# Performance work log

Measured on AMD Instinct MI355X. Metric: run time of the kernel, lower is better.

Reference implementation:

```python
import jax, jax.numpy as jnp
import numpy as np

N_NODES = 100000
N_EDGES = 3200000
F_IN = 128
F_OUT = 128


def setup_inputs() -> dict:
    key = jax.random.key(0)
    ks = jax.random.split(key, 6)
    stdv = 1.0 / np.sqrt(F_OUT)
    return {
        "x": jax.random.normal(ks[0], (N_NODES, F_IN), dtype=jnp.float32),
        "weight": jax.random.uniform(ks[1], (F_IN, F_OUT), minval=-stdv, maxval=stdv, dtype=jnp.float32),
        "bias": jax.random.uniform(ks[2], (F_OUT,), minval=-stdv, maxval=stdv, dtype=jnp.float32),
        "edge_src": jax.random.randint(ks[3], (N_EDGES,), 0, N_NODES, dtype=jnp.int32),
        "edge_dst": jax.random.randint(ks[4], (N_EDGES,), 0, N_NODES, dtype=jnp.int32),
        "edge_weight": jax.random.uniform(ks[5], (N_EDGES,), dtype=jnp.float32),
    }


def reference(x, weight, bias, edge_src, edge_dst, edge_weight):
    # Dense feature transform: support = X @ W  -> [N, F_OUT]
    support = jnp.matmul(x, weight)
    # Sparse adjacency aggregation (SpMM): out[d] = sum_e A[d, s_e] * support[s_e]
    msgs = support[edge_src] * edge_weight[:, None]  # [E, F_OUT]
    out = jax.ops.segment_sum(msgs, edge_dst, num_segments=N_NODES)
    return out + bias
```

## Files before the change

### kernel.cpp

```cpp
#include <hip/hip_runtime.h>

#define F 128
#define NB 64
#define MAXB 2048
#define NCHUNK 256
#define BCAP 3072

typedef __bf16 bf16x8 __attribute__((ext_vector_type(8)));
typedef unsigned short u16x8 __attribute__((ext_vector_type(8)));
typedef float f32x4 __attribute__((ext_vector_type(4)));

static __device__ __forceinline__ unsigned short f2bf(float f) {
    unsigned u = __float_as_uint(f);
    unsigned r = (u + 0x7FFF + ((u >> 16) & 1)) >> 16;
    return (unsigned short)r;
}

__global__ __launch_bounds__(256) void gemm_mfma_kernel(const float* __restrict__ X,
                                                        const float* __restrict__ W,
                                                        unsigned short* __restrict__ Sb,
                                                        int n_nodes) {
    __shared__ unsigned short WT[F * F];
    int t = threadIdx.x;
    {
        int f = t >> 1, half = t & 1;
#pragma unroll
        for (int j = 0; j < 8; ++j) {
            int k0 = half * 64 + j * 8;
            u16x8 pk;
#pragma unroll
            for (int i = 0; i < 8; ++i) pk[i] = f2bf(W[(size_t)(k0 + i) * F + f]);
            int byte = f * 256 + ((k0 * 2) ^ ((f & 7) << 4));
            *(u16x8*)((char*)WT + byte) = pk;
        }
    }
    __syncthreads();

    int w = t >> 6, l = t & 63;
    int lr = l & 15, lg = l >> 4;
    int rowBase = blockIdx.x * 128 + w * 32;

    f32x4 acc[2][8] = {};
    int r0 = rowBase + lr;
    int r1 = rowBase + 16 + lr;
    if (r0 >= n_nodes) r0 = n_nodes - 1;
    if (r1 >= n_nodes) r1 = n_nodes - 1;
    const float* a0p = X + (size_t)r0 * F + lg * 8;
    const float* a1p = X + (size_t)r1 * F + lg * 8;

#pragma unroll
    for (int kt = 0; kt < 4; ++kt) {
        float4 x0 = *(const float4*)(a0p + kt * 32);
        float4 x1 = *(const float4*)(a0p + kt * 32 + 4);
        u16x8 au;
        au[0] = f2bf(x0.x); au[1] = f2bf(x0.y); au[2] = f2bf(x0.z); au[3] = f2bf(x0.w);
        au[4] = f2bf(x1.x); au[5] = f2bf(x1.y); au[6] = f2bf(x1.z); au[7] = f2bf(x1.w);
        bf16x8 a0 = __builtin_bit_cast(bf16x8, au);
        float4 y0 = *(const float4*)(a1p + kt * 32);
        float4 y1 = *(const float4*)(a1p + kt * 32 + 4);
        au[0] = f2bf(y0.x); au[1] = f2bf(y0.y); au[2] = f2bf(y0.z); au[3] = f2bf(y0.w);
        au[4] = f2bf(y1.x); au[5] = f2bf(y1.y); au[6] = f2bf(y1.z); au[7] = f2bf(y1.w);
        bf16x8 a1 = __builtin_bit_cast(bf16x8, au);
#pragma unroll
        for (int ct = 0; ct < 8; ++ct) {
            int f = ct * 16 + lr;
            int byte = f * 256 + (((kt * 32 + lg * 8) * 2) ^ ((f & 7) << 4));
            bf16x8 b = *(bf16x8*)((char*)WT + byte);
            acc[0][ct] = __builtin_amdgcn_mfma_f32_16x16x32_bf16(a0, b, acc[0][ct], 0, 0, 0);
            acc[1][ct] = __builtin_amdgcn_mfma_f32_16x16x32_bf16(a1, b, acc[1][ct], 0, 0, 0);
        }
    }

#pragma unroll
    for (int tile = 0; tile < 2; ++tile) {
#pragma unroll
        for (int ct = 0; ct < 8; ++ct) {
            int col = ct * 16 + lr;
#pragma unroll
            for (int j = 0; j < 4; ++j) {
                int row = rowBase + tile * 16 + lg * 4 + j;
                if (row < n_nodes) Sb[(size_t)row * F + col] = f2bf(acc[tile][ct][j]);
            }
        }
    }
}

__global__ __launch_bounds__(256) void chunk_hist_kernel(const int* __restrict__ edst,
                                                         int* __restrict__ counts,
                                                         int* __restrict__ bcnt,
                                                         int n_edges, int nbuck, int epc) {
    __shared__ int h[MAXB];
    int c = blockIdx.x, t = threadIdx.x;
    for (int i = t; i < nbuck; i += 256) h[i] = 0;
    __syncthreads();
    int beg = c * epc, end = min(n_edges, beg + epc);
    for (int e = beg + t; e < end; e += 256) {
        atomicAdd(&h[edst[e] >> 6], 1);
    }
    __syncthreads();
    for (int i = t; i < nbuck; i += 256) {
        int v = h[i];
        counts[(size_t)c * nbuck + i] = v;
        if (v) __hip_atomic_fetch_add(&bcnt[i], v, __ATOMIC_RELAXED, __HIP_MEMORY_SCOPE_AGENT);
    }
}

__global__ __launch_bounds__(256) void bscan_kernel(const int* __restrict__ bcnt,
                                                    int* __restrict__ bstart, int nbuck) {
    __shared__ int tsum[256];
    int t = threadIdx.x;
    const int EPT = MAXB / 256;
    int base = t * EPT;
    int v[EPT];
    int s = 0;
#pragma unroll
    for (int i = 0; i < EPT; ++i) {
        int idx = base + i;
        v[i] = (idx < nbuck) ? bcnt[idx] : 0;
        s += v[i];
    }
    tsum[t] = s;
    __syncthreads();
    for (int off = 1; off < 256; off <<= 1) {
        int x = (t >= off) ? tsum[t - off] : 0;
        __syncthreads();
        tsum[t] += x;
        __syncthreads();
    }
    int run = tsum[t] - s;
#pragma unroll
    for (int i = 0; i < EPT; ++i) {
        int idx = base + i;
        if (idx < nbuck) {
            bstart[idx] = run;
            run += v[i];
        }
    }
    if (t == 255) bstart[nbuck] = run;
}

__global__ __launch_bounds__(256) void chunk_offs_kernel(const int* __restrict__ counts,
                                                         const int* __restrict__ bstart,
                                                         int* __restrict__ offs, int nbuck) {
    __shared__ int part[4][64];
    int t = threadIdx.x;
    int q = t >> 6, bb = t & 63;
    int b = blockIdx.x * 64 + bb;
    int s = 0;
    if (b < nbuck) {
        for (int c = q * 64; c < q * 64 + 64; ++c) s += counts[(size_t)c * nbuck + b];
    }
    part[q][bb] = s;
    __syncthreads();
    if (b < nbuck) {
        int run = bstart[b];
        for (int qq = 0; qq < q; ++qq) run += part[qq][bb];
        for (int c = q * 64; c < q * 64 + 64; ++c) {
            size_t idx = (size_t)c * nbuck + b;
            offs[idx] = run;
            run += counts[idx];
        }
    }
}

__global__ __launch_bounds__(256) void chunk_scatter_kernel(const int* __restrict__ esrc,
                                                            const int* __restrict__ edst,
                                                            const float* __restrict__ ew,
                                                            const int* __restrict__ offs,
                                                            int2* __restrict__ ebuf,
                                                            int n_edges, int nbuck, int epc) {
    __shared__ int lcur[MAXB];
    int c = blockIdx.x, t = threadIdx.x;
    for (int i = t; i < nbuck; i += 256) lcur[i] = offs[(size_t)c * nbuck + i];
    __syncthreads();
    int beg = c * epc, end = min(n_edges, beg + epc);
    for (int e = beg + t; e < end; e += 256) {
        int d = edst[e];
        int pos = atomicAdd(&lcur[d >> 6], 1);
        int2 p;
        p.x = esrc[e] | ((d & (NB - 1)) << 20);
        p.y = __float_as_int(ew[e]);
        ebuf[pos] = p;
    }
}

__global__ __launch_bounds__(256) void local_sort_kernel(const int2* __restrict__ ebuf,
                                                         const int* __restrict__ bstart,
                                                         unsigned* __restrict__ csr,
                                                         int* __restrict__ rowst,
                                                         int* __restrict__ cnt_out, int n_nodes) {
    __shared__ int lcnt[NB];
    __shared__ int lcur[NB];
    __shared__ int2 se[BCAP];
    int b = blockIdx.x, t = threadIdx.x;
    int beg = bstart[b], end = bstart[b + 1];
    int num = end - beg;
    bool inl = num <= BCAP;

    if (t < NB) lcnt[t] = 0;
    __syncthreads();

    for (int i = t; i < num; i += 256) {
        int2 p = ebuf[beg + i];
        if (inl) se[i] = p;
        atomicAdd(&lcnt[(p.x >> 20) & (NB - 1)], 1);
    }
    __syncthreads();

    if (t < NB) {
        int v = lcnt[t];
        int inc = v;
#pragma unroll
        for (int off = 1; off < NB; off <<= 1) {
            int up = __shfl_up(inc, off, NB);
            if (t >= off) inc += up;
        }
        int excl = inc - v;
        lcur[t] = excl;
        int node = b * NB + t;
        if (node < n_nodes) {
            rowst[node] = beg + excl;
            cnt_out[node] = v;
        }
    }
    __syncthreads();

    for (int i = t; i < num; i += 256) {
        int2 p = inl ? se[i] : ebuf[beg + i];
        int dl = (p.x >> 20) & (NB - 1);
        int pos = beg + atomicAdd(&lcur[dl], 1);
        float wv = __int_as_float(p.y);
        unsigned wfix = (unsigned)(wv * 4095.0f + 0.5f);
        if (wfix > 4095u) wfix = 4095u;
        csr[pos] = (unsigned)(p.x & 0xFFFFF) | (wfix << 20);
    }
}

__global__ __launch_bounds__(256) void gather_kernel(const unsigned short* __restrict__ Sb,
                                                     const unsigned* __restrict__ csr,
                                                     const int* __restrict__ rowst,
                                                     const int* __restrict__ cnt,
                                                     const float* __restrict__ bias,
                                                     float* __restrict__ out, int n_nodes) {
    int node = blockIdx.x * 4 + (threadIdx.x >> 6);
    if (node >= n_nodes) return;
    int lane = threadIdx.x & 63;
    int half = lane >> 5, l32 = lane & 31;

    int beg = rowst[node];
    int num = cnt[node];
    int last = beg + num - 1;

    float4 acc = {0.f, 0.f, 0.f, 0.f};
    const unsigned short* sbp = Sb + l32 * 4;
    const float WSCALE = 1.0f / 4095.0f;

    int i = 0;
    for (; i + 16 <= num; i += 16) {
        unsigned long long g[8];
        float wt[8];
#pragma unroll
        for (int j = 0; j < 8; ++j) {
            unsigned p = csr[beg + i + 2 * j + half];
            g[j] = *(const unsigned long long*)(sbp + (size_t)(p & 0xFFFFFu) * F);
            wt[j] = (float)(p >> 20) * WSCALE;
        }
#pragma unroll
        for (int j = 0; j < 8; ++j) {
            unsigned lo = (unsigned)g[j], hi = (unsigned)(g[j] >> 32);
            acc.x += wt[j] * __uint_as_float(lo << 16);
            acc.y += wt[j] * __uint_as_float(lo & 0xFFFF0000u);
            acc.z += wt[j] * __uint_as_float(hi << 16);
            acc.w += wt[j] * __uint_as_float(hi & 0xFFFF0000u);
        }
    }
    for (; i < num; i += 2) {
        bool live = (i + half) < num;
        unsigned p = csr[live ? beg + i + half : last];
        float wt = live ? (float)(p >> 20) * WSCALE : 0.f;
        unsigned long long g = *(const unsigned long long*)(sbp + (size_t)(p & 0xFFFFFu) * F);
        unsigned lo = (unsigned)g, hi = (unsigned)(g >> 32);
        acc.x += wt * __uint_as_float(lo << 16);
        acc.y += wt * __uint_as_float(lo & 0xFFFF0000u);
        acc.z += wt * __uint_as_float(hi << 16);
        acc.w += wt * __uint_as_float(hi & 0xFFFF0000u);
    }

    acc.x += __shfl_xor(acc.x, 32);
    acc.y += __shfl_xor(acc.y, 32);
    acc.z += __shfl_xor(acc.z, 32);
    acc.w += __shfl_xor(acc.w, 32);

    if (half == 0) {
        float4 bi = *(const float4*)&bias[l32 * 4];
        acc.x += bi.x; acc.y += bi.y; acc.z += bi.z; acc.w += bi.w;
        *(float4*)&out[(size_t)node * F + l32 * 4] = acc;
    }
}

__global__ __launch_bounds__(256) void init_out_kernel(float* __restrict__ out,
                                                       const float* __restrict__ bias,
                                                       int n_nodes) {
    int idx = blockIdx.x * blockDim.x + threadIdx.x;
    int total = n_nodes * F;
    if (idx < total) out[idx] = bias[idx & (F - 1)];
}

__global__ __launch_bounds__(256) void scatter_edges_kernel(const unsigned short* __restrict__ Sb,
                                                            const int* __restrict__ esrc,
                                                            const int* __restrict__ edst,
                                                            const float* __restrict__ ew,
                                                            float* __restrict__ out,
                                                            int n_edges) {
    long long idx = (long long)blockIdx.x * blockDim.x + threadIdx.x;
    int e = (int)(idx >> 5);
    if (e >= n_edges) return;
    int fbase = ((int)idx & 31) * 4;
    int s = esrc[e];
    int d = edst[e];
    float w = ew[e];
    ushort4 v = *(const ushort4*)&Sb[(size_t)s * F + fbase];
    float* o = out + (size_t)d * F + fbase;
    __hip_atomic_fetch_add(&o[0], w * __uint_as_float((unsigned)v.x << 16), __ATOMIC_RELAXED, __HIP_MEMORY_SCOPE_AGENT);
    __hip_atomic_fetch_add(&o[1], w * __uint_as_float((unsigned)v.y << 16), __ATOMIC_RELAXED, __HIP_MEMORY_SCOPE_AGENT);
    __hip_atomic_fetch_add(&o[2], w * __uint_as_float((unsigned)v.z << 16), __ATOMIC_RELAXED, __HIP_MEMORY_SCOPE_AGENT);
    __hip_atomic_fetch_add(&o[3], w * __uint_as_float((unsigned)v.w << 16), __ATOMIC_RELAXED, __HIP_MEMORY_SCOPE_AGENT);
}

extern "C" void kernel_launch(void* const* d_in, const int* in_sizes, int n_in,
                              void* d_out, int out_size, void* d_ws, size_t ws_size,
                              hipStream_t stream) {
    const float* x    = (const float*)d_in[0];
    const float* w    = (const float*)d_in[1];
    const float* bias = (const float*)d_in[2];
    const int*   esrc = (const int*)d_in[3];
    const int*   edst = (const int*)d_in[4];
    const float* ew   = (const float*)d_in[5];
    float* out = (float*)d_out;

    int n_nodes = in_sizes[0] / F;
    int n_edges = in_sizes[3];
    int nbuck = (n_nodes + NB - 1) / NB;
    int epc = (n_edges + NCHUNK - 1) / NCHUNK;

    size_t off = 0;
    auto carve = [&](size_t bytes) -> void* {
        void* p = (char*)d_ws + off;
        off += (bytes + 255) & ~(size_t)255;
        return p;
    };
    unsigned short* Sb    = (unsigned short*)carve((size_t)n_nodes * F * sizeof(unsigned short));
    int2*           ebuf  = (int2*)carve((size_t)n_edges * sizeof(int2));
    unsigned*       csr   = (unsigned*)carve((size_t)n_edges * sizeof(unsigned));
    int*            bcnt  = (int*)carve((size_t)nbuck * sizeof(int));
    int*            bst   = (int*)carve((size_t)(nbuck + 1) * sizeof(int));
    int*            rowst = (int*)carve((size_t)n_nodes * sizeof(int));
    int*            ncnt  = (int*)carve((size_t)n_nodes * sizeof(int));
    int*            counts = (int*)carve((size_t)NCHUNK * nbuck * sizeof(int));
    int*            offs   = (int*)carve((size_t)NCHUNK * nbuck * sizeof(int));
    bool ok = (off <= ws_size) && (nbuck <= MAXB) && (n_nodes < (1 << 20));

    gemm_mfma_kernel<<<(n_nodes + 127) / 128, 256, 0, stream>>>(x, w, Sb, n_nodes);

    if (ok) {
        hipMemsetAsync(bcnt, 0, (size_t)nbuck * sizeof(int), stream);
        chunk_hist_kernel<<<NCHUNK, 256, 0, stream>>>(edst, counts, bcnt, n_edges, nbuck, epc);
        bscan_kernel<<<1, 256, 0, stream>>>(bcnt, bst, nbuck);
        chunk_offs_kernel<<<(nbuck + 63) / 64, 256, 0, stream>>>(counts, bst, offs, nbuck);
        chunk_scatter_kernel<<<NCHUNK, 256, 0, stream>>>(esrc, edst, ew, offs, ebuf,
                                                         n_edges, nbuck, epc);
        local_sort_kernel<<<nbuck, 256, 0, stream>>>(ebuf, bst, csr, rowst, ncnt, n_nodes);
        gather_kernel<<<(n_nodes + 3) / 4, 256, 0, stream>>>(Sb, csr, rowst, ncnt, bias, out,
                                                             n_nodes);
    } else {
        int total = n_nodes * F;
        init_out_kernel<<<(total + 255) / 256, 256, 0, stream>>>(out, bias, n_nodes);
        long long t2 = (long long)n_edges * 32;
        scatter_edges_kernel<<<(int)((t2 + 255) / 256), 256, 0, stream>>>(Sb, esrc, edst, ew, out,
                                                                          n_edges);
    }
}
```

Baseline: 248.7 us.

## Fuse local bucket sort with gather and vectorize edge loads in hist/scatter

Merges the per-bucket local sort and the per-node gather into one kernel. The sorted CSR records stay in shared memory, and each block then aggregates its 64 nodes with four waves handling 16 nodes each. This removes a kernel launch, the global CSR write and re-read, and the rowstart/count arrays. It also vectorizes the edge loads in the histogram and scatter kernels to int4, rounding chunk size to a multiple of 4. The cost is lower gather parallelism: 1563 blocks each process 64 nodes serially per wave, so occupancy drops and load balance gets worse, and shared memory use per block rises.

```diff
diff --git a/kernel.cpp b/kernel.cpp
--- a/kernel.cpp
+++ b/kernel.cpp
@@ -94,8 +94,16 @@
     for (int i = t; i < nbuck; i += 256) h[i] = 0;
     __syncthreads();
     int beg = c * epc, end = min(n_edges, beg + epc);
-    for (int e = beg + t; e < end; e += 256) {
-        atomicAdd(&h[edst[e] >> 6], 1);
+    for (int e0 = beg + t * 4; e0 < end; e0 += 1024) {
+        if (e0 + 4 <= end) {
+            int4 d4 = *(const int4*)&edst[e0];
+            atomicAdd(&h[d4.x >> 6], 1);
+            atomicAdd(&h[d4.y >> 6], 1);
+            atomicAdd(&h[d4.z >> 6], 1);
+            atomicAdd(&h[d4.w >> 6], 1);
+        } else {
+            for (int e = e0; e < end; ++e) atomicAdd(&h[edst[e] >> 6], 1);
+        }
     }
     __syncthreads();
     for (int i = t; i < nbuck; i += 256) {
@@ -174,41 +182,61 @@
     for (int i = t; i < nbuck; i += 256) lcur[i] = offs[(size_t)c * nbuck + i];
     __syncthreads();
     int beg = c * epc, end = min(n_edges, beg + epc);
-    for (int e = beg + t; e < end; e += 256) {
-        int d = edst[e];
-        int pos = atomicAdd(&lcur[d >> 6], 1);
-        int2 p;
-        p.x = esrc[e] | ((d & (NB - 1)) << 20);
-        p.y = __float_as_int(ew[e]);
-        ebuf[pos] = p;
-    }
-}
-
-__global__ __launch_bounds__(256) void local_sort_kernel(const int2* __restrict__ ebuf,
-                                                         const int* __restrict__ bstart,
-                                                         unsigned* __restrict__ csr,
-                                                         int* __restrict__ rowst,
-                                                         int* __restrict__ cnt_out, int n_nodes) {
-    __shared__ int lcnt[NB];
+    for (int e0 = beg + t * 4; e0 < end; e0 += 1024) {
+        if (e0 + 4 <= end) {
+            int4 s4 = *(const int4*)&esrc[e0];
+            int4 d4 = *(const int4*)&edst[e0];
+            float4 w4 = *(const float4*)&ew[e0];
+            int2 p;
+            int pos;
+            pos = atomicAdd(&lcur[d4.x >> 6], 1);
+            p.x = s4.x | ((d4.x & (NB - 1)) << 20); p.y = __float_as_int(w4.x); ebuf[pos] = p;
+            pos = atomicAdd(&lcur[d4.y >> 6], 1);
+            p.x = s4.y | ((d4.y & (NB - 1)) << 20); p.y = __float_as_int(w4.y); ebuf[pos] = p;
+            pos = atomicAdd(&lcur[d4.z >> 6], 1);
+            p.x = s4.z | ((d4.z & (NB - 1)) << 20); p.y = __float_as_int(w4.z); ebuf[pos] = p;
+            pos = atomicAdd(&lcur[d4.w >> 6], 1);
+            p.x = s4.w | ((d4.w & (NB - 1)) << 20); p.y = __float_as_int(w4.w); ebuf[pos] = p;
+        } else {
+            for (int e = e0; e < end; ++e) {
+                int d = edst[e];
+                int pos = atomicAdd(&lcur[d >> 6], 1);
+                int2 p;
+                p.x = esrc[e] | ((d & (NB - 1)) << 20);
+                p.y = __float_as_int(ew[e]);
+                ebuf[pos] = p;
+            }
+        }
+    }
+}
+
+__global__ __launch_bounds__(256) void sort_gather_kernel(const unsigned short* __restrict__ Sb,
+                                                          const int2* __restrict__ ebuf,
+                                                          const int* __restrict__ bstart,
+                                                          unsigned* __restrict__ csr,
+                                                          const float* __restrict__ bias,
+                                                          float* __restrict__ out, int n_nodes) {
+    __shared__ int2 se[BCAP];
+    __shared__ unsigned sorted[BCAP];
+    __shared__ int lrs[NB + 1];
     __shared__ int lcur[NB];
-    __shared__ int2 se[BCAP];
     int b = blockIdx.x, t = threadIdx.x;
     int beg = bstart[b], end = bstart[b + 1];
     int num = end - beg;
     bool inl = num <= BCAP;
 
-    if (t < NB) lcnt[t] = 0;
+    if (t < NB) lcur[t] = 0;
     __syncthreads();
 
     for (int i = t; i < num; i += 256) {
         int2 p = ebuf[beg + i];
         if (inl) se[i] = p;
-        atomicAdd(&lcnt[(p.x >> 20) & (NB - 1)], 1);
+        atomicAdd(&lcur[(p.x >> 20) & (NB - 1)], 1);
     }
     __syncthreads();
 
     if (t < NB) {
-        int v = lcnt[t];
+        int v = lcur[t];
         int inc = v;
 #pragma unroll
         for (int off = 1; off < NB; off <<= 1) {
@@ -216,85 +244,82 @@
             if (t >= off) inc += up;
         }
         int excl = inc - v;
+        lrs[t] = excl;
         lcur[t] = excl;
-        int node = b * NB + t;
-        if (node < n_nodes) {
-            rowst[node] = beg + excl;
-            cnt_out[node] = v;
-        }
+        if (t == NB - 1) lrs[NB] = inc;
     }
     __syncthreads();
 
     for (int i = t; i < num; i += 256) {
         int2 p = inl ? se[i] : ebuf[beg + i];
         int dl = (p.x >> 20) & (NB - 1);
-        int pos = beg + atomicAdd(&lcur[dl], 1);
+        int pos = atomicAdd(&lcur[dl], 1);
         float wv = __int_as_float(p.y);
         unsigned wfix = (unsigned)(wv * 4095.0f + 0.5f);
         if (wfix > 4095u) wfix = 4095u;
-        csr[pos] = (unsigned)(p.x & 0xFFFFF) | (wfix << 20);
-    }
-}
-
-__global__ __launch_bounds__(256) void gather_kernel(const unsigned short* __restrict__ Sb,
-                                                     const unsigned* __restrict__ csr,
-                                                     const int* __restrict__ rowst,
-                                                     const int* __restrict__ cnt,
-                                                     const float* __restrict__ bias,
-                                                     float* __restrict__ out, int n_nodes) {
-    int node = blockIdx.x * 4 + (threadIdx.x >> 6);
-    if (node >= n_nodes) return;
-    int lane = threadIdx.x & 63;
+        unsigned rec = (unsigned)(p.x & 0xFFFFF) | (wfix << 20);
+        if (inl) sorted[pos] = rec;
+        else csr[beg + pos] = rec;
+    }
+    __syncthreads();
+
+    int w = t >> 6, lane = t & 63;
     int half = lane >> 5, l32 = lane & 31;
-
-    int beg = rowst[node];
-    int num = cnt[node];
-    int last = beg + num - 1;
-
-    float4 acc = {0.f, 0.f, 0.f, 0.f};
     const unsigned short* sbp = Sb + l32 * 4;
     const float WSCALE = 1.0f / 4095.0f;
 
-    int i = 0;
-    for (; i + 16 <= num; i += 16) {
-        unsigned long long g[8];
-        float wt[8];
-#pragma unroll
-        for (int j = 0; j < 8; ++j) {
-            unsigned p = csr[beg + i + 2 * j + half];
-            g[j] = *(const unsigned long long*)(sbp + (size_t)(p & 0xFFFFFu) * F);
-            wt[j] = (float)(p >> 20) * WSCALE;
-        }
-#pragma unroll
-        for (int j = 0; j < 8; ++j) {
-            unsigned lo = (unsigned)g[j], hi = (unsigned)(g[j] >> 32);
-            acc.x += wt[j] * __uint_as_float(lo << 16);
-            acc.y += wt[j] * __uint_as_float(lo & 0xFFFF0000u);
-            acc.z += wt[j] * __uint_as_float(hi << 16);
-            acc.w += wt[j] * __uint_as_float(hi & 0xFFFF0000u);
-        }
-    }
-    for (; i < num; i += 2) {
-        bool live = (i + half) < num;
-        unsigned p = csr[live ? beg + i + half : last];
-        float wt = live ? (float)(p >> 20) * WSCALE : 0.f;
-        unsigned long long g = *(const unsigned long long*)(sbp + (size_t)(p & 0xFFFFFu) * F);
-        unsigned lo = (unsigned)g, hi = (unsigned)(g >> 32);
-        acc.x += wt * __uint_as_float(lo << 16);
-        acc.y += wt * __uint_as_float(lo & 0xFFFF0000u);
-        acc.z += wt * __uint_as_float(hi << 16);
-        acc.w += wt * __uint_as_float(hi & 0xFFFF0000u);
-    }
-
-    acc.x += __shfl_xor(acc.x, 32);
-    acc.y += __shfl_xor(acc.y, 32);
-    acc.z += __shfl_xor(acc.z, 32);
-    acc.w += __shfl_xor(acc.w, 32);
-
-    if (half == 0) {
-        float4 bi = *(const float4*)&bias[l32 * 4];
-        acc.x += bi.x; acc.y += bi.y; acc.z += bi.z; acc.w += bi.w;
-        *(float4*)&out[(size_t)node * F + l32 * 4] = acc;
+    for (int k = 0; k < 16; ++k) {
+        int node_l = w * 16 + k;
+        int node = b * NB + node_l;
+        if (node >= n_nodes) break;
+        int s0 = lrs[node_l];
+        int cntn = lrs[node_l + 1] - s0;
+        int last = s0 + cntn - 1;
+
+        float4 acc = {0.f, 0.f, 0.f, 0.f};
+        int i = 0;
+        for (; i + 16 <= cntn; i += 16) {
+            unsigned long long g[8];
+            float wt[8];
+#pragma unroll
+            for (int j = 0; j < 8; ++j) {
+                int idx = s0 + i + 2 * j + half;
+                unsigned p = inl ? sorted[idx] : csr[beg + idx];
+                g[j] = *(const unsigned long long*)(sbp + (size_t)(p & 0xFFFFFu) * F);
+                wt[j] = (float)(p >> 20) * WSCALE;
+            }
+#pragma unroll
+            for (int j = 0; j < 8; ++j) {
+                unsigned lo = (unsigned)g[j], hi = (unsigned)(g[j] >> 32);
+                acc.x += wt[j] * __uint_as_float(lo << 16);
+                acc.y += wt[j] * __uint_as_float(lo & 0xFFFF0000u);
+                acc.z += wt[j] * __uint_as_float(hi << 16);
+                acc.w += wt[j] * __uint_as_float(hi & 0xFFFF0000u);
+            }
+        }
+        for (; i < cntn; i += 2) {
+            bool live = (i + half) < cntn;
+            int idx = live ? s0 + i + half : last;
+            unsigned p = inl ? sorted[idx] : csr[beg + idx];
+            float wt = live ? (float)(p >> 20) * WSCALE : 0.f;
+            unsigned long long g = *(const unsigned long long*)(sbp + (size_t)(p & 0xFFFFFu) * F);
+            unsigned lo = (unsigned)g, hi = (unsigned)(g >> 32);
+            acc.x += wt * __uint_as_float(lo << 16);
+            acc.y += wt * __uint_as_float(lo & 0xFFFF0000u);
+            acc.z += wt * __uint_as_float(hi << 16);
+            acc.w += wt * __uint_as_float(hi & 0xFFFF0000u);
+        }
+
+        acc.x += __shfl_xor(acc.x, 32);
+        acc.y += __shfl_xor(acc.y, 32);
+        acc.z += __shfl_xor(acc.z, 32);
+        acc.w += __shfl_xor(acc.w, 32);
+
+        if (half == 0) {
+            float4 bi = *(const float4*)&bias[l32 * 4];
+            acc.x += bi.x; acc.y += bi.y; acc.z += bi.z; acc.w += bi.w;
+            *(float4*)&out[(size_t)node * F + l32 * 4] = acc;
+        }
     }
 }
 
@@ -341,7 +366,7 @@
     int n_nodes = in_sizes[0] / F;
     int n_edges = in_sizes[3];
     int nbuck = (n_nodes + NB - 1) / NB;
-    int epc = (n_edges + NCHUNK - 1) / NCHUNK;
+    int epc = ((n_edges + NCHUNK - 1) / NCHUNK + 3) & ~3;
 
     size_t off = 0;
     auto carve = [&](size_t bytes) -> void* {
@@ -354,8 +379,6 @@
     unsigned*       csr   = (unsigned*)carve((size_t)n_edges * sizeof(unsigned));
     int*            bcnt  = (int*)carve((size_t)nbuck * sizeof(int));
     int*            bst   = (int*)carve((size_t)(nbuck + 1) * sizeof(int));
-    int*            rowst = (int*)carve((size_t)n_nodes * sizeof(int));
-    int*            ncnt  = (int*)carve((size_t)n_nodes * sizeof(int));
     int*            counts = (int*)carve((size_t)NCHUNK * nbuck * sizeof(int));
     int*            offs   = (int*)carve((size_t)NCHUNK * nbuck * sizeof(int));
     bool ok = (off <= ws_size) && (nbuck <= MAXB) && (n_nodes < (1 << 20));
@@ -369,9 +392,7 @@
         chunk_offs_kernel<<<(nbuck + 63) / 64, 256, 0, stream>>>(counts, bst, offs, nbuck);
         chunk_scatter_kernel<<<NCHUNK, 256, 0, stream>>>(esrc, edst, ew, offs, ebuf,
                                                          n_edges, nbuck, epc);
-        local_sort_kernel<<<nbuck, 256, 0, stream>>>(ebuf, bst, csr, rowst, ncnt, n_nodes);
-        gather_kernel<<<(n_nodes + 3) / 4, 256, 0, stream>>>(Sb, csr, rowst, ncnt, bias, out,
-                                                             n_nodes);
+        sort_gather_kernel<<<nbuck, 256, 0, stream>>>(Sb, ebuf, bst, csr, bias, out, n_nodes);
     } else {
         int total = n_nodes * F;
         init_out_kernel<<<(total + 255) / 256, 256, 0, stream>>>(out, bias, n_nodes);
```

Result: slower. 326.1 us (+31.1%).

## Fuse GEMM and edge histogram into one launch; vectorize edge loads

Applied to the files above, without the earlier changes.

Merges the dense GEMM and the chunk histogram into one kernel, where the first blocks do the GEMM and the rest build histograms, so the two independent stages run at the same time and one launch is removed. The histogram and scatter loops now read edge arrays as int4/float4, with edges per chunk rounded up to a multiple of 4 to keep the loads aligned. The fallback path gets a simple scalar GEMM kernel. Shared memory is sized for the GEMM's 32KB W tile, which may limit how many histogram blocks fit on a CU.

```diff
diff --git a/kernel.cpp b/kernel.cpp
--- a/kernel.cpp
+++ b/kernel.cpp
@@ -16,92 +16,104 @@
     return (unsigned short)r;
 }
 
-__global__ __launch_bounds__(256) void gemm_mfma_kernel(const float* __restrict__ X,
+__global__ __launch_bounds__(256) void gemm_hist_kernel(const float* __restrict__ X,
                                                         const float* __restrict__ W,
                                                         unsigned short* __restrict__ Sb,
-                                                        int n_nodes) {
-    __shared__ unsigned short WT[F * F];
+                                                        int n_nodes,
+                                                        const int* __restrict__ edst,
+                                                        int* __restrict__ counts,
+                                                        int* __restrict__ bcnt,
+                                                        int n_edges, int nbuck, int epc,
+                                                        int ngemm) {
+    __shared__ char smem[F * F * 2];
     int t = threadIdx.x;
-    {
-        int f = t >> 1, half = t & 1;
-#pragma unroll
-        for (int j = 0; j < 8; ++j) {
-            int k0 = half * 64 + j * 8;
-            u16x8 pk;
-#pragma unroll
-            for (int i = 0; i < 8; ++i) pk[i] = f2bf(W[(size_t)(k0 + i) * F + f]);
-            int byte = f * 256 + ((k0 * 2) ^ ((f & 7) << 4));
-            *(u16x8*)((char*)WT + byte) = pk;
-        }
-    }
-    __syncthreads();
-
-    int w = t >> 6, l = t & 63;
-    int lr = l & 15, lg = l >> 4;
-    int rowBase = blockIdx.x * 128 + w * 32;
-
-    f32x4 acc[2][8] = {};
-    int r0 = rowBase + lr;
-    int r1 = rowBase + 16 + lr;
-    if (r0 >= n_nodes) r0 = n_nodes - 1;
-    if (r1 >= n_nodes) r1 = n_nodes - 1;
-    const float* a0p = X + (size_t)r0 * F + lg * 8;
-    const float* a1p = X + (size_t)r1 * F + lg * 8;
-
-#pragma unroll
-    for (int kt = 0; kt < 4; ++kt) {
-        float4 x0 = *(const float4*)(a0p + kt * 32);
-        float4 x1 = *(const float4*)(a0p + kt * 32 + 4);
-        u16x8 au;
-        au[0] = f2bf(x0.x); au[1] = f2bf(x0.y); au[2] = f2bf(x0.z); au[3] = f2bf(x0.w);
-        au[4] = f2bf(x1.x); au[5] = f2bf(x1.y); au[6] = f2bf(x1.z); au[7] = f2bf(x1.w);
-        bf16x8 a0 = __builtin_bit_cast(bf16x8, au);
-        float4 y0 = *(const float4*)(a1p + kt * 32);
-        float4 y1 = *(const float4*)(a1p + kt * 32 + 4);
-        au[0] = f2bf(y0.x); au[1] = f2bf(y0.y); au[2] = f2bf(y0.z); au[3] = f2bf(y0.w);
-        au[4] = f2bf(y1.x); au[5] = f2bf(y1.y); au[6] = f2bf(y1.z); au[7] = f2bf(y1.w);
-        bf16x8 a1 = __builtin_bit_cast(bf16x8, au);
-#pragma unroll
-        for (int ct = 0; ct < 8; ++ct) {
-            int f = ct * 16 + lr;
-            int byte = f * 256 + (((kt * 32 + lg * 8) * 2) ^ ((f & 7) << 4));
-            bf16x8 b = *(bf16x8*)((char*)WT + byte);
-            acc[0][ct] = __builtin_amdgcn_mfma_f32_16x16x32_bf16(a0, b, acc[0][ct], 0, 0, 0);
-            acc[1][ct] = __builtin_amdgcn_mfma_f32_16x16x32_bf16(a1, b, acc[1][ct], 0, 0, 0);
-        }
-    }
-
-#pragma unroll
-    for (int tile = 0; tile < 2; ++tile) {
-#pragma unroll
-        for (int ct = 0; ct < 8; ++ct) {
-            int col = ct * 16 + lr;
-#pragma unroll
-            for (int j = 0; j < 4; ++j) {
-                int row = rowBase + tile * 16 + lg * 4 + j;
-                if (row < n_nodes) Sb[(size_t)row * F + col] = f2bf(acc[tile][ct][j]);
+
+    if ((int)blockIdx.x < ngemm) {
+        unsigned short* WT = (unsigned short*)smem;
+        {
+            int f = t >> 1, half = t & 1;
+#pragma unroll
+            for (int j = 0; j < 8; ++j) {
+                int k0 = half * 64 + j * 8;
+                u16x8 pk;
+#pragma unroll
+                for (int i = 0; i < 8; ++i) pk[i] = f2bf(W[(size_t)(k0 + i) * F + f]);
+                int byte = f * 256 + ((k0 * 2) ^ ((f & 7) << 4));
+                *(u16x8*)((char*)WT + byte) = pk;
             }
         }
-    }
-}
-
-__global__ __launch_bounds__(256) void chunk_hist_kernel(const int* __restrict__ edst,
-                                                         int* __restrict__ counts,
-                                                         int* __restrict__ bcnt,
-                                                         int n_edges, int nbuck, int epc) {
-    __shared__ int h[MAXB];
-    int c = blockIdx.x, t = threadIdx.x;
-    for (int i = t; i < nbuck; i += 256) h[i] = 0;
-    __syncthreads();
-    int beg = c * epc, end = min(n_edges, beg + epc);
-    for (int e = beg + t; e < end; e += 256) {
-        atomicAdd(&h[edst[e] >> 6], 1);
-    }
-    __syncthreads();
-    for (int i = t; i < nbuck; i += 256) {
-        int v = h[i];
-        counts[(size_t)c * nbuck + i] = v;
-        if (v) __hip_atomic_fetch_add(&bcnt[i], v, __ATOMIC_RELAXED, __HIP_MEMORY_SCOPE_AGENT);
+        __syncthreads();
+
+        int w = t >> 6, l = t & 63;
+        int lr = l & 15, lg = l >> 4;
+        int rowBase = blockIdx.x * 128 + w * 32;
+
+        f32x4 acc[2][8] = {};
+        int r0 = rowBase + lr;
+        int r1 = rowBase + 16 + lr;
+        if (r0 >= n_nodes) r0 = n_nodes - 1;
+        if (r1 >= n_nodes) r1 = n_nodes - 1;
+        const float* a0p = X + (size_t)r0 * F + lg * 8;
+        const float* a1p = X + (size_t)r1 * F + lg * 8;
+
+#pragma unroll
+        for (int kt = 0; kt < 4; ++kt) {
+            float4 x0 = *(const float4*)(a0p + kt * 32);
+            float4 x1 = *(const float4*)(a0p + kt * 32 + 4);
+            u16x8 au;
+            au[0] = f2bf(x0.x); au[1] = f2bf(x0.y); au[2] = f2bf(x0.z); au[3] = f2bf(x0.w);
+            au[4] = f2bf(x1.x); au[5] = f2bf(x1.y); au[6] = f2bf(x1.z); au[7] = f2bf(x1.w);
+            bf16x8 a0 = __builtin_bit_cast(bf16x8, au);
+            float4 y0 = *(const float4*)(a1p + kt * 32);
+            float4 y1 = *(const float4*)(a1p + kt * 32 + 4);
+            au[0] = f2bf(y0.x); au[1] = f2bf(y0.y); au[2] = f2bf(y0.z); au[3] = f2bf(y0.w);
+            au[4] = f2bf(y1.x); au[5] = f2bf(y1.y); au[6] = f2bf(y1.z); au[7] = f2bf(y1.w);
+            bf16x8 a1 = __builtin_bit_cast(bf16x8, au);
+#pragma unroll
+            for (int ct = 0; ct < 8; ++ct) {
+                int f = ct * 16 + lr;
+                int byte = f * 256 + (((kt * 32 + lg * 8) * 2) ^ ((f & 7) << 4));
+                bf16x8 bfr = *(bf16x8*)((char*)WT + byte);
+                acc[0][ct] = __builtin_amdgcn_mfma_f32_16x16x32_bf16(a0, bfr, acc[0][ct], 0, 0, 0);
+                acc[1][ct] = __builtin_amdgcn_mfma_f32_16x16x32_bf16(a1, bfr, acc[1][ct], 0, 0, 0);
+            }
+        }
+
+#pragma unroll
+        for (int tile = 0; tile < 2; ++tile) {
+#pragma unroll
+            for (int ct = 0; ct < 8; ++ct) {
+                int col = ct * 16 + lr;
+#pragma unroll
+                for (int j = 0; j < 4; ++j) {
+                    int row = rowBase + tile * 16 + lg * 4 + j;
+                    if (row < n_nodes) Sb[(size_t)row * F + col] = f2bf(acc[tile][ct][j]);
+                }
+            }
+        }
+    } else {
+        int* h = (int*)smem;
+        int c = blockIdx.x - ngemm;
+        for (int i = t; i < nbuck; i += 256) h[i] = 0;
+        __syncthreads();
+        int beg = c * epc, end = min(n_edges, beg + epc);
+        for (int e0 = beg + t * 4; e0 < end; e0 += 1024) {
+            if (e0 + 4 <= end) {
+                int4 d4 = *(const int4*)&edst[e0];
+                atomicAdd(&h[d4.x >> 6], 1);
+                atomicAdd(&h[d4.y >> 6], 1);
+                atomicAdd(&h[d4.z >> 6], 1);
+                atomicAdd(&h[d4.w >> 6], 1);
+            } else {
+                for (int e = e0; e < end; ++e) atomicAdd(&h[edst[e] >> 6], 1);
+            }
+        }
+        __syncthreads();
+        for (int i = t; i < nbuck; i += 256) {
+            int v = h[i];
+            counts[(size_t)c * nbuck + i] = v;
+            if (v) __hip_atomic_fetch_add(&bcnt[i], v, __ATOMIC_RELAXED, __HIP_MEMORY_SCOPE_AGENT);
+        }
     }
 }
 
@@ -174,13 +186,31 @@
     for (int i = t; i < nbuck; i += 256) lcur[i] = offs[(size_t)c * nbuck + i];
     __syncthreads();
     int beg = c * epc, end = min(n_edges, beg + epc);
-    for (int e = beg + t; e < end; e += 256) {
-        int d = edst[e];
-        int pos = atomicAdd(&lcur[d >> 6], 1);
-        int2 p;
-        p.x = esrc[e] | ((d & (NB - 1)) << 20);
-        p.y = __float_as_int(ew[e]);
-        ebuf[pos] = p;
+    for (int e0 = beg + t * 4; e0 < end; e0 += 1024) {
+        if (e0 + 4 <= end) {
+            int4 s4 = *(const int4*)&esrc[e0];
+            int4 d4 = *(const int4*)&edst[e0];
+            float4 w4 = *(const float4*)&ew[e0];
+            int2 p;
+            int pos;
+            pos = atomicAdd(&lcur[d4.x >> 6], 1);
+            p.x = s4.x | ((d4.x & (NB - 1)) << 20); p.y = __float_as_int(w4.x); ebuf[pos] = p;
+            pos = atomicAdd(&lcur[d4.y >> 6], 1);
+            p.x = s4.y | ((d4.y & (NB - 1)) << 20); p.y = __float_as_int(w4.y); ebuf[pos] = p;
+            pos = atomicAdd(&lcur[d4.z >> 6], 1);
+            p.x = s4.z | ((d4.z & (NB - 1)) << 20); p.y = __float_as_int(w4.z); ebuf[pos] = p;
+            pos = atomicAdd(&lcur[d4.w >> 6], 1);
+            p.x = s4.w | ((d4.w & (NB - 1)) << 20); p.y = __float_as_int(w4.w); ebuf[pos] = p;
+        } else {
+            for (int e = e0; e < end; ++e) {
+                int d = edst[e];
+                int pos = atomicAdd(&lcur[d >> 6], 1);
+                int2 p;
+                p.x = esrc[e] | ((d & (NB - 1)) << 20);
+                p.y = __float_as_int(ew[e]);
+                ebuf[pos] = p;
+            }
+        }
     }
 }
 
@@ -304,6 +334,28 @@
     int idx = blockIdx.x * blockDim.x + threadIdx.x;
     int total = n_nodes * F;
     if (idx < total) out[idx] = bias[idx & (F - 1)];
+}
+
+__global__ __launch_bounds__(256) void gemm_fb_kernel(const float* __restrict__ X,
+                                                      const float* __restrict__ W,
+                                                      unsigned short* __restrict__ Sb,
+                                                      int n_nodes) {
+    __shared__ float Wl[F * F / 2];
+    (void)Wl;
+    int idx = blockIdx.x * blockDim.x + threadIdx.x;
+    int row = idx >> 5;
+    int fb = (idx & 31) * 4;
+    if (row >= n_nodes) return;
+    const float* xr = X + (size_t)row * F;
+    float a0 = 0, a1 = 0, a2 = 0, a3 = 0;
+    for (int k = 0; k < F; ++k) {
+        float xv = xr[k];
+        const float* wr = W + (size_t)k * F + fb;
+        a0 += xv * wr[0]; a1 += xv * wr[1]; a2 += xv * wr[2]; a3 += xv * wr[3];
+    }
+    ushort4 res;
+    res.x = f2bf(a0); res.y = f2bf(a1); res.z = f2bf(a2); res.w = f2bf(a3);
+    *(ushort4*)&Sb[(size_t)row * F + fb] = res;
 }
 
 __global__ __launch_bounds__(256) void scatter_edges_kernel(const unsigned short* __restrict__ Sb,
@@ -341,7 +393,7 @@
     int n_nodes = in_sizes[0] / F;
     int n_edges = in_sizes[3];
     int nbuck = (n_nodes + NB - 1) / NB;
-    int epc = (n_edges + NCHUNK - 1) / NCHUNK;
+    int epc = ((n_edges + NCHUNK - 1) / NCHUNK + 3) & ~3;
 
     size_t off = 0;
     auto carve = [&](size_t bytes) -> void* {
@@ -360,11 +412,11 @@
     int*            offs   = (int*)carve((size_t)NCHUNK * nbuck * sizeof(int));
     bool ok = (off <= ws_size) && (nbuck <= MAXB) && (n_nodes < (1 << 20));
 
-    gemm_mfma_kernel<<<(n_nodes + 127) / 128, 256, 0, stream>>>(x, w, Sb, n_nodes);
-
     if (ok) {
+        int ngemm = (n_nodes + 127) / 128;
         hipMemsetAsync(bcnt, 0, (size_t)nbuck * sizeof(int), stream);
-        chunk_hist_kernel<<<NCHUNK, 256, 0, stream>>>(edst, counts, bcnt, n_edges, nbuck, epc);
+        gemm_hist_kernel<<<ngemm + NCHUNK, 256, 0, stream>>>(x, w, Sb, n_nodes, edst, counts,
+                                                             bcnt, n_edges, nbuck, epc, ngemm);
         bscan_kernel<<<1, 256, 0, stream>>>(bcnt, bst, nbuck);
         chunk_offs_kernel<<<(nbuck + 63) / 64, 256, 0, stream>>>(counts, bst, offs, nbuck);
         chunk_scatter_kernel<<<NCHUNK, 256, 0, stream>>>(esrc, edst, ew, offs, ebuf,
@@ -373,6 +425,7 @@
         gather_kernel<<<(n_nodes + 3) / 4, 256, 0, stream>>>(Sb, csr, rowst, ncnt, bias, out,
                                                              n_nodes);
     } else {
+        gemm_fb_kernel<<<(n_nodes * 32 + 255) / 256, 256, 0, stream>>>(x, w, Sb, n_nodes);
         int total = n_nodes * F;
         init_out_kernel<<<(total + 255) / 256, 256, 0, stream>>>(out, bias, n_nodes);
         long long t2 = (long long)n_edges * 32;
```

Measured after the change: 231.6 us. -6.9%, faster.
